# Kernel tuning notes

Measured on AMD Instinct MI355X. Metric: run time of the kernel, lower is better.

The kernel has to match this reference:

```python
import jax, jax.numpy as jnp
import numpy as np

B, N, K, C_IN, M, C_OUT = 2, 20000, 16, 128, 9, 128


def setup_inputs() -> dict:
    key = jax.random.key(0)
    k1, k2, k3, k4, k5, k6 = jax.random.split(key, 6)
    x = jax.random.normal(k1, (B, N, C_IN), dtype=jnp.float32)
    # 0 == "no neighbor" (maps to the prepended zero row); valid ids are 1..N
    adj = jax.random.randint(k2, (N, K), 0, N, dtype=jnp.int32)
    W = jax.random.uniform(k3, (M, C_OUT, C_IN), jnp.float32, -0.05, 0.05)
    b = jax.random.uniform(k4, (C_OUT,), jnp.float32, -0.05, 0.05)
    u = jax.random.uniform(k5, (M, C_IN), jnp.float32, -0.05, 0.05)
    c = jax.random.uniform(k6, (M,), jnp.float32, -0.05, 0.05)
    return {"x": x, "adj": adj, "W": W, "b": b, "u": u, "c": c}


def reference(x, adj, W, b, u, c):
    Bb, Nn, Cin = x.shape
    # prepend zero row so adj==0 gathers zeros (padding neighbor)
    xp = jnp.concatenate([jnp.zeros((Bb, 1, Cin), x.dtype), x], axis=1)
    patches = xp[:, adj]                      # [B, N, K, C] neighbor features
    # pseudo-coordinate differences -> soft assignment over M kernels
    diff = x[:, :, None, :] - patches          # [B, N, K, C]
    logits = jnp.einsum('bnkc,mc->bnkm', diff, u) + c
    q = jax.nn.softmax(logits, axis=-1)        # softmax over M (last axis)
    # inverse neighbor count (0 where the node has no neighbors)
    deg = jnp.count_nonzero(adj, axis=1).astype(x.dtype)        # [N]
    deg_inv = jnp.where(deg > 0, 1.0 / jnp.maximum(deg, 1.0), 0.0)
    # out[b,n,o] = deg_inv[n] * sum_{k,m} q[b,n,k,m] * (W[m] @ x_nbr)[o]
    msg = jnp.einsum('bnkm,moc,bnkc->bno', q, W, patches)        # [B, N, O]
    return msg * deg_inv[None, :, None] + b
```

## Files before the change

### kernel.cpp

```cpp
#include <hip/hip_runtime.h>
#include <hip/hip_bf16.h>

#define NB 2
#define NN 20000
#define NKN 16
#define NC 128
#define NM 9
#define NO 128
#define NR (NB*NN)
#define KK (NM*NC)
#define NKC (KK/32)
#define NPB 16
#define YS 12
#define YB (NR/64)

typedef short bf16x8 __attribute__((ext_vector_type(8)));
typedef float f32x4 __attribute__((ext_vector_type(4)));
typedef float f32x2 __attribute__((ext_vector_type(2)));
typedef unsigned short u16x8 __attribute__((ext_vector_type(8)));

__device__ inline f32x2 bfpair(unsigned int w) {
    union { unsigned int u; float f; } lo, hi;
    lo.u = w << 16; hi.u = w & 0xFFFF0000u;
    return (f32x2){lo.f, hi.f};
}

__global__ __launch_bounds__(256) void prep_kernel(const float* __restrict__ x,
                                                   const float* __restrict__ u,
                                                   const float* __restrict__ W,
                                                   float* __restrict__ y,
                                                   __hip_bfloat16* __restrict__ xb,
                                                   __hip_bfloat16* __restrict__ Wg,
                                                   int use_xb) {
    int tid = threadIdx.x;
    if (blockIdx.x < YB) {
        int wave = tid >> 6, lane = tid & 63;
        int lr = lane & 15, quad = lane >> 4;
        int node0 = blockIdx.x * 64 + wave * 16;
        long xbase = (long)(node0 + lr) * NC;

        bf16x8 afr[4];
        #pragma unroll
        for (int kc = 0; kc < 4; kc++) {
            const float* px = x + xbase + kc * 32 + quad * 8;
            float4 a0 = *(const float4*)px;
            float4 a1 = *(const float4*)(px + 4);
            union { bf16x8 v; unsigned short s[8]; __hip_bfloat16 h[8]; } af;
            af.h[0] = __float2bfloat16(a0.x); af.h[1] = __float2bfloat16(a0.y);
            af.h[2] = __float2bfloat16(a0.z); af.h[3] = __float2bfloat16(a0.w);
            af.h[4] = __float2bfloat16(a1.x); af.h[5] = __float2bfloat16(a1.y);
            af.h[6] = __float2bfloat16(a1.z); af.h[7] = __float2bfloat16(a1.w);
            afr[kc] = af.v;
            if (use_xb)
                *(u16x8*)((unsigned short*)xb + xbase + kc * 32 + quad * 8) =
                    *(u16x8*)&af.v;
        }
        int cs = (lr < NM) ? lr : 0;
        float fz = (lr < NM) ? 1.f : 0.f;
        f32x4 acc = (f32x4){0.f, 0.f, 0.f, 0.f};
        #pragma unroll
        for (int kc = 0; kc < 4; kc++) {
            const float* pu = u + cs * NC + kc * 32 + quad * 8;
            float4 b0 = *(const float4*)pu;
            float4 b1 = *(const float4*)(pu + 4);
            union { bf16x8 v; __hip_bfloat16 h[8]; } bf;
            bf.h[0] = __float2bfloat16(b0.x * fz); bf.h[1] = __float2bfloat16(b0.y * fz);
            bf.h[2] = __float2bfloat16(b0.z * fz); bf.h[3] = __float2bfloat16(b0.w * fz);
            bf.h[4] = __float2bfloat16(b1.x * fz); bf.h[5] = __float2bfloat16(b1.y * fz);
            bf.h[6] = __float2bfloat16(b1.z * fz); bf.h[7] = __float2bfloat16(b1.w * fz);
            acc = __builtin_amdgcn_mfma_f32_16x16x32_bf16(afr[kc], bf.v, acc, 0, 0, 0);
        }
        if (lr < NM) {
            #pragma unroll
            for (int r = 0; r < 4; r++)
                y[(long)(node0 + quad * 4 + r) * YS + lr] = acc[r];
        }
    } else {
        int t = (blockIdx.x - YB) * 256 + tid;
        int c = t & 127;
        int o = (t >> 7) & 127;
        int m = t >> 14;
        int kk = m * 128 + c;
        float v = W[m * 16384 + o * 128 + c];
        Wg[((kk >> 5) * 128 + o) * 32 + (kk & 31)] = __float2bfloat16(v);
    }
}

template<bool BF16G>
__global__ __launch_bounds__(256, 4) void fused_kernel(const float* __restrict__ x,
                                                       const __hip_bfloat16* __restrict__ xb,
                                                       const int* __restrict__ adj,
                                                       const float* __restrict__ y,
                                                       const float* __restrict__ cv,
                                                       const __hip_bfloat16* __restrict__ Wg,
                                                       const float* __restrict__ bv,
                                                       float* __restrict__ out) {
    __shared__ __align__(16) short s_S[NPB * KK];

    int tid = threadIdx.x;
    int node0 = blockIdx.x * NPB;
    int b = node0 / NN;
    int n0 = node0 - b * NN;
    int ln = tid >> 4, k = tid & 15;

    float* qb_ = (float*)((char*)s_S + ln * (KK * 2) + ((ln & 7) << 4));

    const int* arow = adj + (n0 + ln) * NKN;
    int a = arow[k];
    int4 r0 = *(const int4*)arow;
    int4 r1 = *(const int4*)(arow + 4);
    int4 r2 = *(const int4*)(arow + 8);
    int4 r3 = *(const int4*)(arow + 12);

    const float* yn = y + (long)(node0 + ln) * YS;
    const float* ya = y + (long)(b * NN + ((a > 0) ? a - 1 : 0)) * YS;
    float4 yn0 = *(const float4*)yn;
    float4 yn1 = *(const float4*)(yn + 4);
    float  yn8 = yn[8];
    float4 ya0 = *(const float4*)ya;
    float4 ya1 = *(const float4*)(ya + 4);
    float  ya8 = ya[8];

    int idx[NKN]; int d = 0;
    #define PUT(J, V) { int aa = (V); d += (aa > 0); idx[J] = (aa > 0) ? aa - 1 : 0; }
    PUT(0, r0.x)  PUT(1, r0.y)  PUT(2, r0.z)  PUT(3, r0.w)
    PUT(4, r1.x)  PUT(5, r1.y)  PUT(6, r1.z)  PUT(7, r1.w)
    PUT(8, r2.x)  PUT(9, r2.y)  PUT(10, r2.z) PUT(11, r2.w)
    PUT(12, r3.x) PUT(13, r3.y) PUT(14, r3.z) PUT(15, r3.w)
    #undef PUT
    float di = (d > 0) ? 1.f / (float)d : 0.f;

    int c8 = k << 3;
    uint4 pw0[8];
    if (BF16G) {
        #pragma unroll
        for (int j = 0; j < 8; j++)
            pw0[j] = *(const uint4*)((const unsigned short*)xb +
                                     (long)(b * NN + idx[j]) * NC + c8);
    }

    {
        float sel = (a > 0) ? 1.f : 0.f;
        float l[NM];
        l[0] = yn0.x - sel * ya0.x + cv[0];
        l[1] = yn0.y - sel * ya0.y + cv[1];
        l[2] = yn0.z - sel * ya0.z + cv[2];
        l[3] = yn0.w - sel * ya0.w + cv[3];
        l[4] = yn1.x - sel * ya1.x + cv[4];
        l[5] = yn1.y - sel * ya1.y + cv[5];
        l[6] = yn1.z - sel * ya1.z + cv[6];
        l[7] = yn1.w - sel * ya1.w + cv[7];
        l[8] = yn8   - sel * ya8   + cv[8];
        float mx = l[0];
        #pragma unroll
        for (int m = 1; m < NM; m++) mx = fmaxf(mx, l[m]);
        float e[NM]; float sum = 0.f;
        #pragma unroll
        for (int m = 0; m < NM; m++) { e[m] = __expf(l[m] - mx); sum += e[m]; }
        float qs = ((a > 0) ? (1.f / sum) : 0.f) * di;
        #pragma unroll
        for (int m = 0; m < NM; m++) qb_[k * 12 + m] = e[m] * qs;
    }
    asm volatile("s_waitcnt lgkmcnt(0)" ::: "memory");
    __builtin_amdgcn_sched_barrier(0);

    f32x2 s2[NM][4];
    #pragma unroll
    for (int m = 0; m < NM; m++)
        #pragma unroll
        for (int j = 0; j < 4; j++) s2[m][j] = (f32x2){0.f, 0.f};

    #define ACC_ALL(P0, P1, P2, P3, KK2) {                                    \
        const float* qr = qb_ + (KK2) * 12;                                   \
        float4 qa = *(const float4*)qr;                                       \
        float4 qb = *(const float4*)(qr + 4);                                 \
        float  q8 = qr[8];                                                    \
        f32x2 qq;                                                             \
        qq=(f32x2){qa.x,qa.x}; s2[0][0]+=qq*P0; s2[0][1]+=qq*P1; s2[0][2]+=qq*P2; s2[0][3]+=qq*P3; \
        qq=(f32x2){qa.y,qa.y}; s2[1][0]+=qq*P0; s2[1][1]+=qq*P1; s2[1][2]+=qq*P2; s2[1][3]+=qq*P3; \
        qq=(f32x2){qa.z,qa.z}; s2[2][0]+=qq*P0; s2[2][1]+=qq*P1; s2[2][2]+=qq*P2; s2[2][3]+=qq*P3; \
        qq=(f32x2){qa.w,qa.w}; s2[3][0]+=qq*P0; s2[3][1]+=qq*P1; s2[3][2]+=qq*P2; s2[3][3]+=qq*P3; \
        qq=(f32x2){qb.x,qb.x}; s2[4][0]+=qq*P0; s2[4][1]+=qq*P1; s2[4][2]+=qq*P2; s2[4][3]+=qq*P3; \
        qq=(f32x2){qb.y,qb.y}; s2[5][0]+=qq*P0; s2[5][1]+=qq*P1; s2[5][2]+=qq*P2; s2[5][3]+=qq*P3; \
        qq=(f32x2){qb.z,qb.z}; s2[6][0]+=qq*P0; s2[6][1]+=qq*P1; s2[6][2]+=qq*P2; s2[6][3]+=qq*P3; \
        qq=(f32x2){qb.w,qb.w}; s2[7][0]+=qq*P0; s2[7][1]+=qq*P1; s2[7][2]+=qq*P2; s2[7][3]+=qq*P3; \
        qq=(f32x2){q8,q8};     s2[8][0]+=qq*P0; s2[8][1]+=qq*P1; s2[8][2]+=qq*P2; s2[8][3]+=qq*P3; }

    if (BF16G) {
        uint4 pw1[8];
        #pragma unroll
        for (int j = 0; j < 8; j++)
            pw1[j] = *(const uint4*)((const unsigned short*)xb +
                                     (long)(b * NN + idx[8 + j]) * NC + c8);
        #pragma unroll
        for (int j = 0; j < 8; j++) {
            f32x2 p0 = bfpair(pw0[j].x), p1 = bfpair(pw0[j].y);
            f32x2 p2 = bfpair(pw0[j].z), p3 = bfpair(pw0[j].w);
            ACC_ALL(p0, p1, p2, p3, j)
        }
        #pragma unroll
        for (int j = 0; j < 8; j++) {
            f32x2 p0 = bfpair(pw1[j].x), p1 = bfpair(pw1[j].y);
            f32x2 p2 = bfpair(pw1[j].z), p3 = bfpair(pw1[j].w);
            ACC_ALL(p0, p1, p2, p3, 8 + j)
        }
    } else {
        #pragma unroll
        for (int g = 0; g < NKN / 4; g++) {
            float4 fa[4], fb[4];
            #pragma unroll
            for (int j = 0; j < 4; j++) {
                const float* px = x + (long)(b * NN + idx[g * 4 + j]) * NC + c8;
                fa[j] = *(const float4*)px;
                fb[j] = *(const float4*)(px + 4);
            }
            #pragma unroll
            for (int j = 0; j < 4; j++) {
                f32x2 p0 = (f32x2){fa[j].x, fa[j].y}, p1 = (f32x2){fa[j].z, fa[j].w};
                f32x2 p2 = (f32x2){fb[j].x, fb[j].y}, p3 = (f32x2){fb[j].z, fb[j].w};
                ACC_ALL(p0, p1, p2, p3, g * 4 + j)
            }
        }
    }
    #undef ACC_ALL

    #pragma unroll
    for (int m = 0; m < NM; m++) {
        u16x8 ov;
        #pragma unroll
        for (int j = 0; j < 4; j++) {
            union { unsigned short h; __hip_bfloat16 bb; } c0, c1;
            c0.bb = __float2bfloat16(s2[m][j][0]);
            c1.bb = __float2bfloat16(s2[m][j][1]);
            ov[j * 2]     = c0.h;
            ov[j * 2 + 1] = c1.h;
        }
        int g = m * 16 + k;
        int gs = g ^ (ln & 7);
        *(u16x8*)(&s_S[ln * KK + gs * 8]) = ov;
    }

    int wave = tid >> 6;
    int lane = tid & 63;
    int lr = lane & 15;
    int quad = lane >> 4;
    const short* wg = reinterpret_cast<const short*>(Wg);
    int col0 = wave * 16 + lr;
    int col1 = col0 + 64;
    float bb0 = bv[col0];
    float bb1 = bv[col1];
    bf16x8 pf0 = *(const bf16x8*)(wg + (wave * 16 + lr) * 32 + quad * 8);
    bf16x8 pf1 = *(const bf16x8*)(wg + ((wave + 4) * 16 + lr) * 32 + quad * 8);

    __syncthreads();

    f32x4 acc0 = (f32x4){0.f, 0.f, 0.f, 0.f};
    f32x4 acc1 = (f32x4){0.f, 0.f, 0.f, 0.f};

    {
        int gs = quad ^ (lr & 7);
        bf16x8 a0 = *(const bf16x8*)(&s_S[lr * KK + gs * 8]);
        acc0 = __builtin_amdgcn_mfma_f32_16x16x32_bf16(a0, pf0, acc0, 0, 0, 0);
        acc1 = __builtin_amdgcn_mfma_f32_16x16x32_bf16(a0, pf1, acc1, 0, 0, 0);
    }
    #pragma unroll 7
    for (int kc = 1; kc < NKC; kc++) {
        int g = kc * 4 + quad;
        int gs = g ^ (lr & 7);
        bf16x8 a0 = *(const bf16x8*)(&s_S[lr * KK + gs * 8]);
        bf16x8 bf0 = *(const bf16x8*)(wg + ((kc * 128) + wave * 16 + lr) * 32 + quad * 8);
        bf16x8 bf1 = *(const bf16x8*)(wg + ((kc * 128) + (wave + 4) * 16 + lr) * 32 + quad * 8);
        acc0 = __builtin_amdgcn_mfma_f32_16x16x32_bf16(a0, bf0, acc0, 0, 0, 0);
        acc1 = __builtin_amdgcn_mfma_f32_16x16x32_bf16(a0, bf1, acc1, 0, 0, 0);
    }

    int rbase = node0 + quad * 4;
    #pragma unroll
    for (int r = 0; r < 4; r++) {
        out[(long)(rbase + r) * NO + col0] = acc0[r] + bb0;
        out[(long)(rbase + r) * NO + col1] = acc1[r] + bb1;
    }
}

extern "C" void kernel_launch(void* const* d_in, const int* in_sizes, int n_in,
                              void* d_out, int out_size, void* d_ws, size_t ws_size,
                              hipStream_t stream) {
    const float* x   = (const float*)d_in[0];
    const int*   adj = (const int*)  d_in[1];
    const float* W   = (const float*)d_in[2];
    const float* bv  = (const float*)d_in[3];
    const float* u   = (const float*)d_in[4];
    const float* cv  = (const float*)d_in[5];
    float* out = (float*)d_out;

    char* ws = (char*)d_ws;
    float* y = (float*)ws;
    __hip_bfloat16* Wg = (__hip_bfloat16*)(ws + 1920000);
    __hip_bfloat16* xb = (__hip_bfloat16*)(ws + 2214912);
    bool use_xb = (ws_size >= (size_t)12454912);

    prep_kernel<<<YB + 576, 256, 0, stream>>>(x, u, W, y, use_xb ? xb : nullptr, Wg,
                                              use_xb ? 1 : 0);
    if (use_xb)
        fused_kernel<true><<<NR / NPB, 256, 0, stream>>>(x, xb, adj, y, cv, Wg, bv, out);
    else
        fused_kernel<false><<<NR / NPB, 256, 0, stream>>>(x, xb, adj, y, cv, Wg, bv, out);
}
```

Before: 139.0 us.

## Process two node tiles per block and overlap next tile's loads with MFMA phase

Each block now handles two 16-node tiles in sequence. It issues the second tile's adjacency reads and first half of neighbor gathers before the first tile's MFMA phase, and loads its y values inside that phase, so memory latency can hide behind matrix work. It also halves the grid size and reuses the preloaded W fragments and bias for both tiles. In exchange it raises register pressure, which could lower occupancy under launch_bounds(256,4), and adds extra barriers.

```diff
diff --git a/kernel.cpp b/kernel.cpp
--- a/kernel.cpp
+++ b/kernel.cpp
@@ -11,6 +11,7 @@
 #define KK (NM*NC)
 #define NKC (KK/32)
 #define NPB 16
+#define NTL 2
 #define YS 12
 #define YB (NR/64)
 
@@ -98,77 +99,90 @@
     __shared__ __align__(16) short s_S[NPB * KK];
 
     int tid = threadIdx.x;
-    int node0 = blockIdx.x * NPB;
-    int b = node0 / NN;
-    int n0 = node0 - b * NN;
+    int tbase = blockIdx.x * (NPB * NTL);
     int ln = tid >> 4, k = tid & 15;
+    int c8 = k << 3;
 
     float* qb_ = (float*)((char*)s_S + ln * (KK * 2) + ((ln & 7) << 4));
 
-    const int* arow = adj + (n0 + ln) * NKN;
-    int a = arow[k];
-    int4 r0 = *(const int4*)arow;
-    int4 r1 = *(const int4*)(arow + 4);
-    int4 r2 = *(const int4*)(arow + 8);
-    int4 r3 = *(const int4*)(arow + 12);
-
-    const float* yn = y + (long)(node0 + ln) * YS;
-    const float* ya = y + (long)(b * NN + ((a > 0) ? a - 1 : 0)) * YS;
-    float4 yn0 = *(const float4*)yn;
-    float4 yn1 = *(const float4*)(yn + 4);
-    float  yn8 = yn[8];
-    float4 ya0 = *(const float4*)ya;
-    float4 ya1 = *(const float4*)(ya + 4);
-    float  ya8 = ya[8];
-
-    int idx[NKN]; int d = 0;
-    #define PUT(J, V) { int aa = (V); d += (aa > 0); idx[J] = (aa > 0) ? aa - 1 : 0; }
-    PUT(0, r0.x)  PUT(1, r0.y)  PUT(2, r0.z)  PUT(3, r0.w)
-    PUT(4, r1.x)  PUT(5, r1.y)  PUT(6, r1.z)  PUT(7, r1.w)
-    PUT(8, r2.x)  PUT(9, r2.y)  PUT(10, r2.z) PUT(11, r2.w)
-    PUT(12, r3.x) PUT(13, r3.y) PUT(14, r3.z) PUT(15, r3.w)
-    #undef PUT
-    float di = (d > 0) ? 1.f / (float)d : 0.f;
-
-    int c8 = k << 3;
-    uint4 pw0[8];
-    if (BF16G) {
-        #pragma unroll
-        for (int j = 0; j < 8; j++)
-            pw0[j] = *(const uint4*)((const unsigned short*)xb +
-                                     (long)(b * NN + idx[j]) * NC + c8);
+    #define DECL_TILE(S) \
+        int node0_##S = tbase + (S) * NPB; \
+        int b_##S = node0_##S / NN; \
+        int n0_##S = node0_##S - b_##S * NN;
+
+    #define PUTV(S, ARR, J, V) \
+        { int aa = (V); d_##S += (aa > 0); ARR##_##S[J] = (aa > 0) ? aa - 1 : 0; }
+
+    #define A_EARLY(S) \
+        const int* arow_##S = adj + (n0_##S + ln) * NKN; \
+        int a_##S = arow_##S[k]; \
+        int4 r0_##S = *(const int4*)arow_##S; \
+        int4 r1_##S = *(const int4*)(arow_##S + 4); \
+        int4 r2_##S = *(const int4*)(arow_##S + 8); \
+        int4 r3_##S = *(const int4*)(arow_##S + 12); \
+        int idxl_##S[8], idxh_##S[8]; int d_##S = 0; \
+        PUTV(S, idxl, 0, r0_##S.x) PUTV(S, idxl, 1, r0_##S.y) \
+        PUTV(S, idxl, 2, r0_##S.z) PUTV(S, idxl, 3, r0_##S.w) \
+        PUTV(S, idxl, 4, r1_##S.x) PUTV(S, idxl, 5, r1_##S.y) \
+        PUTV(S, idxl, 6, r1_##S.z) PUTV(S, idxl, 7, r1_##S.w) \
+        PUTV(S, idxh, 0, r2_##S.x) PUTV(S, idxh, 1, r2_##S.y) \
+        PUTV(S, idxh, 2, r2_##S.z) PUTV(S, idxh, 3, r2_##S.w) \
+        PUTV(S, idxh, 4, r3_##S.x) PUTV(S, idxh, 5, r3_##S.y) \
+        PUTV(S, idxh, 6, r3_##S.z) PUTV(S, idxh, 7, r3_##S.w) \
+        float di_##S = (d_##S > 0) ? 1.f / (float)d_##S : 0.f; \
+        uint4 pw0_##S[8]; \
+        if (BF16G) { \
+            const unsigned short* xbs_ = (const unsigned short*)xb; \
+            long rb_ = (long)b_##S * NN; \
+            pw0_##S[0] = *(const uint4*)(xbs_ + (rb_ + idxl_##S[0]) * NC + c8); \
+            pw0_##S[1] = *(const uint4*)(xbs_ + (rb_ + idxl_##S[1]) * NC + c8); \
+            pw0_##S[2] = *(const uint4*)(xbs_ + (rb_ + idxl_##S[2]) * NC + c8); \
+            pw0_##S[3] = *(const uint4*)(xbs_ + (rb_ + idxl_##S[3]) * NC + c8); \
+            pw0_##S[4] = *(const uint4*)(xbs_ + (rb_ + idxl_##S[4]) * NC + c8); \
+            pw0_##S[5] = *(const uint4*)(xbs_ + (rb_ + idxl_##S[5]) * NC + c8); \
+            pw0_##S[6] = *(const uint4*)(xbs_ + (rb_ + idxl_##S[6]) * NC + c8); \
+            pw0_##S[7] = *(const uint4*)(xbs_ + (rb_ + idxl_##S[7]) * NC + c8); \
+        }
+
+    #define Y_DECL(S) \
+        float4 yn0_##S, yn1_##S, ya0_##S, ya1_##S; \
+        float yn8_##S, ya8_##S;
+
+    #define Y_LOAD(S) { \
+        const float* ynp = y + (long)(node0_##S + ln) * YS; \
+        const float* yap = y + ((long)b_##S * NN + ((a_##S > 0) ? a_##S - 1 : 0)) * YS; \
+        yn0_##S = *(const float4*)ynp; \
+        yn1_##S = *(const float4*)(ynp + 4); \
+        yn8_##S = ynp[8]; \
+        ya0_##S = *(const float4*)yap; \
+        ya1_##S = *(const float4*)(yap + 4); \
+        ya8_##S = yap[8]; \
     }
 
-    {
-        float sel = (a > 0) ? 1.f : 0.f;
-        float l[NM];
-        l[0] = yn0.x - sel * ya0.x + cv[0];
-        l[1] = yn0.y - sel * ya0.y + cv[1];
-        l[2] = yn0.z - sel * ya0.z + cv[2];
-        l[3] = yn0.w - sel * ya0.w + cv[3];
-        l[4] = yn1.x - sel * ya1.x + cv[4];
-        l[5] = yn1.y - sel * ya1.y + cv[5];
-        l[6] = yn1.z - sel * ya1.z + cv[6];
-        l[7] = yn1.w - sel * ya1.w + cv[7];
-        l[8] = yn8   - sel * ya8   + cv[8];
-        float mx = l[0];
-        #pragma unroll
-        for (int m = 1; m < NM; m++) mx = fmaxf(mx, l[m]);
-        float e[NM]; float sum = 0.f;
-        #pragma unroll
-        for (int m = 0; m < NM; m++) { e[m] = __expf(l[m] - mx); sum += e[m]; }
-        float qs = ((a > 0) ? (1.f / sum) : 0.f) * di;
-        #pragma unroll
-        for (int m = 0; m < NM; m++) qb_[k * 12 + m] = e[m] * qs;
-    }
-    asm volatile("s_waitcnt lgkmcnt(0)" ::: "memory");
+    #define SOFTMAX_Q(S) { \
+        float sel = (a_##S > 0) ? 1.f : 0.f; \
+        float l[NM]; \
+        l[0] = yn0_##S.x - sel * ya0_##S.x + cv[0]; \
+        l[1] = yn0_##S.y - sel * ya0_##S.y + cv[1]; \
+        l[2] = yn0_##S.z - sel * ya0_##S.z + cv[2]; \
+        l[3] = yn0_##S.w - sel * ya0_##S.w + cv[3]; \
+        l[4] = yn1_##S.x - sel * ya1_##S.x + cv[4]; \
+        l[5] = yn1_##S.y - sel * ya1_##S.y + cv[5]; \
+        l[6] = yn1_##S.z - sel * ya1_##S.z + cv[6]; \
+        l[7] = yn1_##S.w - sel * ya1_##S.w + cv[7]; \
+        l[8] = yn8_##S   - sel * ya8_##S   + cv[8]; \
+        float mx = l[0]; \
+        _Pragma("unroll") \
+        for (int m = 1; m < NM; m++) mx = fmaxf(mx, l[m]); \
+        float e[NM]; float sum = 0.f; \
+        _Pragma("unroll") \
+        for (int m = 0; m < NM; m++) { e[m] = __expf(l[m] - mx); sum += e[m]; } \
+        float qs = ((a_##S > 0) ? (1.f / sum) : 0.f) * di_##S; \
+        _Pragma("unroll") \
+        for (int m = 0; m < NM; m++) qb_[k * 12 + m] = e[m] * qs; \
+    } \
+    asm volatile("s_waitcnt lgkmcnt(0)" ::: "memory"); \
     __builtin_amdgcn_sched_barrier(0);
-
-    f32x2 s2[NM][4];
-    #pragma unroll
-    for (int m = 0; m < NM; m++)
-        #pragma unroll
-        for (int j = 0; j < 4; j++) s2[m][j] = (f32x2){0.f, 0.f};
 
     #define ACC_ALL(P0, P1, P2, P3, KK2) {                                    \
         const float* qr = qb_ + (KK2) * 12;                                   \
@@ -186,59 +200,114 @@
         qq=(f32x2){qb.w,qb.w}; s2[7][0]+=qq*P0; s2[7][1]+=qq*P1; s2[7][2]+=qq*P2; s2[7][3]+=qq*P3; \
         qq=(f32x2){q8,q8};     s2[8][0]+=qq*P0; s2[8][1]+=qq*P1; s2[8][2]+=qq*P2; s2[8][3]+=qq*P3; }
 
-    if (BF16G) {
-        uint4 pw1[8];
-        #pragma unroll
-        for (int j = 0; j < 8; j++)
-            pw1[j] = *(const uint4*)((const unsigned short*)xb +
-                                     (long)(b * NN + idx[8 + j]) * NC + c8);
-        #pragma unroll
-        for (int j = 0; j < 8; j++) {
-            f32x2 p0 = bfpair(pw0[j].x), p1 = bfpair(pw0[j].y);
-            f32x2 p2 = bfpair(pw0[j].z), p3 = bfpair(pw0[j].w);
-            ACC_ALL(p0, p1, p2, p3, j)
-        }
-        #pragma unroll
-        for (int j = 0; j < 8; j++) {
-            f32x2 p0 = bfpair(pw1[j].x), p1 = bfpair(pw1[j].y);
-            f32x2 p2 = bfpair(pw1[j].z), p3 = bfpair(pw1[j].w);
-            ACC_ALL(p0, p1, p2, p3, 8 + j)
-        }
-    } else {
-        #pragma unroll
-        for (int g = 0; g < NKN / 4; g++) {
-            float4 fa[4], fb[4];
-            #pragma unroll
-            for (int j = 0; j < 4; j++) {
-                const float* px = x + (long)(b * NN + idx[g * 4 + j]) * NC + c8;
-                fa[j] = *(const float4*)px;
-                fb[j] = *(const float4*)(px + 4);
-            }
-            #pragma unroll
-            for (int j = 0; j < 4; j++) {
-                f32x2 p0 = (f32x2){fa[j].x, fa[j].y}, p1 = (f32x2){fa[j].z, fa[j].w};
-                f32x2 p2 = (f32x2){fb[j].x, fb[j].y}, p3 = (f32x2){fb[j].z, fb[j].w};
-                ACC_ALL(p0, p1, p2, p3, g * 4 + j)
-            }
-        }
+    #define ACC_PACK(S) { \
+        _Pragma("unroll") \
+        for (int m = 0; m < NM; m++) { \
+            _Pragma("unroll") \
+            for (int j = 0; j < 4; j++) s2[m][j] = (f32x2){0.f, 0.f}; \
+        } \
+        if (BF16G) { \
+            const unsigned short* xbs_ = (const unsigned short*)xb; \
+            long rb_ = (long)b_##S * NN; \
+            uint4 pw1[8]; \
+            pw1[0] = *(const uint4*)(xbs_ + (rb_ + idxh_##S[0]) * NC + c8); \
+            pw1[1] = *(const uint4*)(xbs_ + (rb_ + idxh_##S[1]) * NC + c8); \
+            pw1[2] = *(const uint4*)(xbs_ + (rb_ + idxh_##S[2]) * NC + c8); \
+            pw1[3] = *(const uint4*)(xbs_ + (rb_ + idxh_##S[3]) * NC + c8); \
+            pw1[4] = *(const uint4*)(xbs_ + (rb_ + idxh_##S[4]) * NC + c8); \
+            pw1[5] = *(const uint4*)(xbs_ + (rb_ + idxh_##S[5]) * NC + c8); \
+            pw1[6] = *(const uint4*)(xbs_ + (rb_ + idxh_##S[6]) * NC + c8); \
+            pw1[7] = *(const uint4*)(xbs_ + (rb_ + idxh_##S[7]) * NC + c8); \
+            _Pragma("unroll") \
+            for (int j = 0; j < 8; j++) { \
+                f32x2 p0 = bfpair(pw0_##S[j].x), p1 = bfpair(pw0_##S[j].y); \
+                f32x2 p2 = bfpair(pw0_##S[j].z), p3 = bfpair(pw0_##S[j].w); \
+                ACC_ALL(p0, p1, p2, p3, j) \
+            } \
+            _Pragma("unroll") \
+            for (int j = 0; j < 8; j++) { \
+                f32x2 p0 = bfpair(pw1[j].x), p1 = bfpair(pw1[j].y); \
+                f32x2 p2 = bfpair(pw1[j].z), p3 = bfpair(pw1[j].w); \
+                ACC_ALL(p0, p1, p2, p3, 8 + j) \
+            } \
+        } else { \
+            long rb_ = (long)b_##S * NN; \
+            _Pragma("unroll") \
+            for (int j = 0; j < 8; j++) { \
+                const float* px = x + (rb_ + idxl_##S[j]) * NC + c8; \
+                float4 fa = *(const float4*)px; \
+                float4 fb = *(const float4*)(px + 4); \
+                f32x2 p0 = (f32x2){fa.x, fa.y}, p1 = (f32x2){fa.z, fa.w}; \
+                f32x2 p2 = (f32x2){fb.x, fb.y}, p3 = (f32x2){fb.z, fb.w}; \
+                ACC_ALL(p0, p1, p2, p3, j) \
+            } \
+            _Pragma("unroll") \
+            for (int j = 0; j < 8; j++) { \
+                const float* px = x + (rb_ + idxh_##S[j]) * NC + c8; \
+                float4 fa = *(const float4*)px; \
+                float4 fb = *(const float4*)(px + 4); \
+                f32x2 p0 = (f32x2){fa.x, fa.y}, p1 = (f32x2){fa.z, fa.w}; \
+                f32x2 p2 = (f32x2){fb.x, fb.y}, p3 = (f32x2){fb.z, fb.w}; \
+                ACC_ALL(p0, p1, p2, p3, 8 + j) \
+            } \
+        } \
+        _Pragma("unroll") \
+        for (int m = 0; m < NM; m++) { \
+            u16x8 ov; \
+            _Pragma("unroll") \
+            for (int j = 0; j < 4; j++) { \
+                union { unsigned short h; __hip_bfloat16 bb; } c0_, c1_; \
+                c0_.bb = __float2bfloat16(s2[m][j][0]); \
+                c1_.bb = __float2bfloat16(s2[m][j][1]); \
+                ov[j * 2]     = c0_.h; \
+                ov[j * 2 + 1] = c1_.h; \
+            } \
+            int g = m * 16 + k; \
+            int gs = g ^ (ln & 7); \
+            *(u16x8*)(&s_S[ln * KK + gs * 8]) = ov; \
+        } \
     }
-    #undef ACC_ALL
-
-    #pragma unroll
-    for (int m = 0; m < NM; m++) {
-        u16x8 ov;
-        #pragma unroll
-        for (int j = 0; j < 4; j++) {
-            union { unsigned short h; __hip_bfloat16 bb; } c0, c1;
-            c0.bb = __float2bfloat16(s2[m][j][0]);
-            c1.bb = __float2bfloat16(s2[m][j][1]);
-            ov[j * 2]     = c0.h;
-            ov[j * 2 + 1] = c1.h;
-        }
-        int g = m * 16 + k;
-        int gs = g ^ (ln & 7);
-        *(u16x8*)(&s_S[ln * KK + gs * 8]) = ov;
+
+    #define B_PHASE(S, ...) { \
+        f32x4 acc0 = (f32x4){0.f, 0.f, 0.f, 0.f}; \
+        f32x4 acc1 = (f32x4){0.f, 0.f, 0.f, 0.f}; \
+        { \
+            int gs = quad ^ (lr & 7); \
+            bf16x8 a0 = *(const bf16x8*)(&s_S[lr * KK + gs * 8]); \
+            acc0 = __builtin_amdgcn_mfma_f32_16x16x32_bf16(a0, pf0, acc0, 0, 0, 0); \
+            acc1 = __builtin_amdgcn_mfma_f32_16x16x32_bf16(a0, pf1, acc1, 0, 0, 0); \
+        } \
+        _Pragma("unroll 7") \
+        for (int kc = 1; kc < NKC; kc++) { \
+            int g = kc * 4 + quad; \
+            int gs = g ^ (lr & 7); \
+            bf16x8 a0 = *(const bf16x8*)(&s_S[lr * KK + gs * 8]); \
+            bf16x8 bf0 = *(const bf16x8*)(wg + ((kc * 128) + wave * 16 + lr) * 32 + quad * 8); \
+            bf16x8 bf1 = *(const bf16x8*)(wg + ((kc * 128) + (wave + 4) * 16 + lr) * 32 + quad * 8); \
+            acc0 = __builtin_amdgcn_mfma_f32_16x16x32_bf16(a0, bf0, acc0, 0, 0, 0); \
+            acc1 = __builtin_amdgcn_mfma_f32_16x16x32_bf16(a0, bf1, acc1, 0, 0, 0); \
+        } \
+        __VA_ARGS__ \
+        int rbase = node0_##S + quad * 4; \
+        _Pragma("unroll") \
+        for (int r = 0; r < 4; r++) { \
+            out[(long)(rbase + r) * NO + col0] = acc0[r] + bb0; \
+            out[(long)(rbase + r) * NO + col1] = acc1[r] + bb1; \
+        } \
     }
+
+    DECL_TILE(0)
+    DECL_TILE(1)
+    f32x2 s2[NM][4];
+
+    A_EARLY(0)
+    Y_DECL(0)
+    Y_LOAD(0)
+    SOFTMAX_Q(0)
+    ACC_PACK(0)
+
+    A_EARLY(1)
+    Y_DECL(1)
 
     int wave = tid >> 6;
     int lane = tid & 63;
@@ -254,32 +323,26 @@
 
     __syncthreads();
 
-    f32x4 acc0 = (f32x4){0.f, 0.f, 0.f, 0.f};
-    f32x4 acc1 = (f32x4){0.f, 0.f, 0.f, 0.f};
-
-    {
-        int gs = quad ^ (lr & 7);
-        bf16x8 a0 = *(const bf16x8*)(&s_S[lr * KK + gs * 8]);
-        acc0 = __builtin_amdgcn_mfma_f32_16x16x32_bf16(a0, pf0, acc0, 0, 0, 0);
-        acc1 = __builtin_amdgcn_mfma_f32_16x16x32_bf16(a0, pf1, acc1, 0, 0, 0);
-    }
-    #pragma unroll 7
-    for (int kc = 1; kc < NKC; kc++) {
-        int g = kc * 4 + quad;
-        int gs = g ^ (lr & 7);
-        bf16x8 a0 = *(const bf16x8*)(&s_S[lr * KK + gs * 8]);
-        bf16x8 bf0 = *(const bf16x8*)(wg + ((kc * 128) + wave * 16 + lr) * 32 + quad * 8);
-        bf16x8 bf1 = *(const bf16x8*)(wg + ((kc * 128) + (wave + 4) * 16 + lr) * 32 + quad * 8);
-        acc0 = __builtin_amdgcn_mfma_f32_16x16x32_bf16(a0, bf0, acc0, 0, 0, 0);
-        acc1 = __builtin_amdgcn_mfma_f32_16x16x32_bf16(a0, bf1, acc1, 0, 0, 0);
-    }
-
-    int rbase = node0 + quad * 4;
-    #pragma unroll
-    for (int r = 0; r < 4; r++) {
-        out[(long)(rbase + r) * NO + col0] = acc0[r] + bb0;
-        out[(long)(rbase + r) * NO + col1] = acc1[r] + bb1;
-    }
+    B_PHASE(0, Y_LOAD(1))
+
+    __syncthreads();
+
+    SOFTMAX_Q(1)
+    ACC_PACK(1)
+
+    __syncthreads();
+
+    B_PHASE(1, ;)
+
+    #undef B_PHASE
+    #undef ACC_PACK
+    #undef ACC_ALL
+    #undef SOFTMAX_Q
+    #undef Y_LOAD
+    #undef Y_DECL
+    #undef A_EARLY
+    #undef PUTV
+    #undef DECL_TILE
 }
 
 extern "C" void kernel_launch(void* const* d_in, const int* in_sizes, int n_in,
@@ -302,7 +365,7 @@
     prep_kernel<<<YB + 576, 256, 0, stream>>>(x, u, W, y, use_xb ? xb : nullptr, Wg,
                                               use_xb ? 1 : 0);
     if (use_xb)
-        fused_kernel<true><<<NR / NPB, 256, 0, stream>>>(x, xb, adj, y, cv, Wg, bv, out);
+        fused_kernel<true><<<NR / (NPB * NTL), 256, 0, stream>>>(x, xb, adj, y, cv, Wg, bv, out);
     else
-        fused_kernel<false><<<NR / NPB, 256, 0, stream>>>(x, xb, adj, y, cv, Wg, bv, out);
+        fused_kernel<false><<<NR / (NPB * NTL), 256, 0, stream>>>(x, xb, adj, y, cv, Wg, bv, out);
 }
```

Measured after the change: 236.2 us. 70.0% more time.
